# Kernel optimization log

Hardware: AMD Instinct MI355X
Metric: run time of the kernel (lower is better)

The kernel has to match this reference:

```python
import jax, jax.numpy as jnp
import numpy as np

T = 1024          # num tokens
H = 2048          # hidden_size
NH = 16           # attention heads
NKV = 4           # kv heads (GQA)
HD = 128          # head_dim
E = 32            # num routed experts
K = 4             # top_k
I = 1024          # moe_intermediate_size
NS = 1            # num_shared_experts
EPS = 1e-6
THETA = 600000.0  # rope base
SCALE = HD ** -0.5


def rmsnorm(x, w):
    return x * jax.lax.rsqrt(jnp.mean(x * x, axis=-1, keepdims=True) + EPS) * w


def rope(x, positions):
    # x: [T, n_heads, HD], neox-style rotation on full head_dim
    half = HD // 2
    inv_freq = 1.0 / (THETA ** (jnp.arange(half, dtype=jnp.float32) / half))
    ang = positions.astype(jnp.float32)[:, None] * inv_freq        # [T, half]
    cos = jnp.cos(ang)[:, None, :]
    sin = jnp.sin(ang)[:, None, :]
    x1, x2 = x[..., :half], x[..., half:]
    return jnp.concatenate([x1 * cos - x2 * sin, x1 * sin + x2 * cos], axis=-1)


def setup_inputs() -> dict:
    key = jax.random.key(0)
    ks = jax.random.split(key, 10)
    s = 0.02
    return {
        "hidden_states": jax.random.normal(ks[0], (T, H), dtype=jnp.float32),
        "positions": jnp.arange(T, dtype=jnp.int32),
        "w_rms1": jnp.ones((H,), jnp.float32),
        "w_rms2": jnp.ones((H,), jnp.float32),
        "w_qkv": jax.random.normal(ks[1], ((NH + 2 * NKV) * HD, H), jnp.float32) * s,
        "w_o": jax.random.normal(ks[2], (H, NH * HD), jnp.float32) * s,
        "w_router": jax.random.normal(ks[3], (E, H), jnp.float32) * s,
        "w1": jax.random.normal(ks[4], (E, H, I), jnp.float32) * s,   # expert gate proj
        "w3": jax.random.normal(ks[5], (E, H, I), jnp.float32) * s,   # expert up proj
        "w2": jax.random.normal(ks[6], (E, I, H), jnp.float32) * s,   # expert down proj
        "ws_gate_up": jax.random.normal(ks[7], (2 * I * NS, H), jnp.float32) * s,
        "ws_down": jax.random.normal(ks[8], (H, I * NS), jnp.float32) * s,
    }


def reference(hidden_states, positions, w_rms1, w_rms2, w_qkv, w_o, w_router,
              w1, w3, w2, ws_gate_up, ws_down):
    x = hidden_states
    # ---- attention block ----
    h = rmsnorm(x, w_rms1)
    qkv = h @ w_qkv.T                                   # [T, (NH+2NKV)*HD]
    q = qkv[:, : NH * HD].reshape(T, NH, HD)
    k = qkv[:, NH * HD : (NH + NKV) * HD].reshape(T, NKV, HD)
    v = qkv[:, (NH + NKV) * HD :].reshape(T, NKV, HD)
    q = rope(q, positions)
    k = rope(k, positions)
    rep = NH // NKV
    k = jnp.repeat(k, rep, axis=1)                      # [T, NH, HD]
    v = jnp.repeat(v, rep, axis=1)
    scores = jnp.einsum("thd,shd->hts", q, k) * SCALE   # [NH, T, T]
    causal = jnp.tril(jnp.ones((T, T), dtype=bool))
    scores = jnp.where(causal, scores, -jnp.inf)
    attn = jax.nn.softmax(scores, axis=-1)
    o = jnp.einsum("hts,shd->thd", attn, v).reshape(T, NH * HD)
    x = x + o @ w_o.T                                   # residual
    # ---- MoE block ----
    h2 = rmsnorm(x, w_rms2)
    # router in fp32 (router_dtype default)
    logits = h2.astype(jnp.float32) @ w_router.T        # [T, E]
    probs = jax.nn.softmax(logits, axis=-1)
    topv, topi = jax.lax.top_k(probs, K)                # [T, K]
    topv = topv / jnp.sum(topv, axis=-1, keepdims=True)  # norm_topk_prob
    combine = jnp.zeros((T, E), jnp.float32).at[jnp.arange(T)[:, None], topi].add(topv)
    combine = combine.astype(h2.dtype)                  # routed_scaling_factor = 1.0
    g = jnp.einsum("th,ehi->tei", h2, w1)               # [T, E, I]
    u = jnp.einsum("th,ehi->tei", h2, w3)
    a = jax.nn.silu(g) * u                              # SiluAndMul
    d = jnp.einsum("tei,eih->teh", a, w2)               # [T, E, H]
    routed = jnp.einsum("teh,te->th", d, combine)
    # shared expert MLP
    gu = h2 @ ws_gate_up.T                              # [T, 2*I*NS]
    gs, us = gu[:, : I * NS], gu[:, I * NS :]
    shared = (jax.nn.silu(gs) * us) @ ws_down.T
    return x + routed + shared
```

## Files before the change

### kernel.cpp

```cpp
#include <hip/hip_runtime.h>
#include <hip/hip_bf16.h>
#include <math.h>
#include <stdint.h>

#define T_ 1024
#define H_ 2048
#define NH_ 16
#define NKV_ 4
#define HD_ 128
#define E_ 32
#define TOPK_ 4
#define I_ 1024
#define QKVN_ 3072
#define EPS_ 1e-6f
#define THETA_ 600000.0f
#define SCALE_ 0.08838834764831845f

typedef unsigned short u16;
typedef u16 u16x4 __attribute__((ext_vector_type(4)));
typedef u16 u16x8 __attribute__((ext_vector_type(8)));
typedef __bf16 bf16x8 __attribute__((ext_vector_type(8)));
typedef float f32x4 __attribute__((ext_vector_type(4)));

__device__ __forceinline__ u16 f2b(float f) {
  unsigned u = __builtin_bit_cast(unsigned, f);
  u += 0x7FFFu + ((u >> 16) & 1u);
  return (u16)(u >> 16);
}
__device__ __forceinline__ float b2f(u16 x) {
  unsigned u = ((unsigned)x) << 16;
  return __builtin_bit_cast(float, u);
}
__device__ __forceinline__ int s2(int i) { return (i ^ (i >> 2)) & 3; }

__device__ __forceinline__ void gload16(const void* g, void* l) {
  __builtin_amdgcn_global_load_lds(
      reinterpret_cast<const __attribute__((address_space(1))) unsigned int*>(
          reinterpret_cast<uintptr_t>(g)),
      reinterpret_cast<__attribute__((address_space(3))) unsigned int*>(
          reinterpret_cast<uintptr_t>(l)),
      16, 0, 0);
}

template<int EPI, bool GATHER>
__global__ __launch_bounds__(512, 8) void moe_gemm_k(
    const u16* __restrict__ A, const float* __restrict__ B, const float* __restrict__ B2,
    float* __restrict__ O1, float* __restrict__ O2,
    int NW, int lda, int ldb, int kchunk,
    const int* __restrict__ eoff, const int* __restrict__ slots,
    const float* __restrict__ slotw, long long sBz)
{
  __shared__ u16 As[2][64 * 32];
  __shared__ u16 Bs[2][128 * 32];

  const int e = blockIdx.y >> 3;
  const int mb = blockIdx.y & 7;
  const int goff = eoff[e];
  const int Mloc = eoff[e + 1] - goff;
  const int m0 = mb * 64;
  if (m0 >= Mloc) return;

  const int xx = blockIdx.x;
  const float* Bp;
  float* Op;
  int n0;
  if constexpr (EPI == 0) {
    int wsel = xx >> 3;
    n0 = (xx & 7) * 128;
    Bp = (wsel ? B2 : B) + (long long)e * sBz;
    Op = wsel ? O2 : O1;
  } else {
    n0 = xx * 128;
    Bp = B + (long long)e * sBz;
    Op = O1;
  }
  const int k0base = blockIdx.z * kchunk;
  const u16* Ae = GATHER ? A : (A + (long long)goff * lda);

  const int tid = threadIdx.x;
  const int lane = tid & 63;
  const int wv = tid >> 6;
  const int wm = wv >> 2, wn = wv & 3;

  const u16* Abase = nullptr;
  if (wv < 4) {
    int r = wv * 16 + (lane >> 2);
    int rr = m0 + r;
    if (rr > Mloc - 1) rr = Mloc - 1;
    long long grow = GATHER ? (long long)slots[goff + rr] : (long long)rr;
    Abase = Ae + grow * (long long)lda + (((lane & 3) ^ s2(r)) << 3);
  }

  const int bn = tid & 127;
  const int bkc = tid >> 7;
  const float* Bbase = Bp + (long long)(bkc << 3) * ldb + n0 + bn;
  const int bws = bn * 32 + ((bkc ^ s2(bn)) << 3);

  float br[8];
  auto loadB = [&](int k0) {
    const float* p = Bbase + (long long)k0 * ldb;
    #pragma unroll
    for (int j = 0; j < 8; ++j) br[j] = p[(long long)j * ldb];
  };
  auto writeB = [&](int bf) {
    u16x8 o;
    #pragma unroll
    for (int j = 0; j < 8; ++j) o[j] = f2b(br[j]);
    *(u16x8*)(&Bs[bf][bws]) = o;
  };
  auto stageA = [&](int bf, int k0) {
    if (wv < 4) gload16(Abase + k0, &As[bf][wv * 512]);
  };

  f32x4 acc[2][2];
  #pragma unroll
  for (int m = 0; m < 2; ++m)
    #pragma unroll
    for (int n = 0; n < 2; ++n)
      acc[m][n] = f32x4{0.f, 0.f, 0.f, 0.f};

  const int kg = lane >> 4;
  const int cr = lane & 15;

  int aoff[2], boff[2];
  #pragma unroll
  for (int m = 0; m < 2; ++m) {
    int r = wm * 32 + m * 16 + cr;
    aoff[m] = r * 32 + ((kg ^ s2(r)) << 3);
  }
  #pragma unroll
  for (int n = 0; n < 2; ++n) {
    int c = wn * 32 + n * 16 + cr;
    boff[n] = c * 32 + ((kg ^ s2(c)) << 3);
  }

  loadB(k0base);
  stageA(0, k0base);
  writeB(0);
  __syncthreads();

  int buf = 0;
  for (int ks = 0; ks < kchunk; ks += 32) {
    bool more = (ks + 32) < kchunk;
    if (more) { loadB(k0base + ks + 32); stageA(buf ^ 1, k0base + ks + 32); }
    const u16* Ap = &As[buf][0];
    const u16* Bq = &Bs[buf][0];
    bf16x8 af[2], bfr[2];
    #pragma unroll
    for (int m = 0; m < 2; ++m)
      af[m] = __builtin_bit_cast(bf16x8, *(const u16x8*)(Ap + aoff[m]));
    #pragma unroll
    for (int n = 0; n < 2; ++n)
      bfr[n] = __builtin_bit_cast(bf16x8, *(const u16x8*)(Bq + boff[n]));
    #pragma unroll
    for (int m = 0; m < 2; ++m)
      #pragma unroll
      for (int n = 0; n < 2; ++n)
        acc[m][n] = __builtin_amdgcn_mfma_f32_16x16x32_bf16(af[m], bfr[n], acc[m][n], 0, 0, 0);
    if (more) writeB(buf ^ 1);
    __syncthreads();
    buf ^= 1;
  }

  const int rq = lane >> 4;
  #pragma unroll
  for (int m = 0; m < 2; ++m) {
    #pragma unroll
    for (int j = 0; j < 4; ++j) {
      int row = m0 + wm * 32 + m * 16 + rq * 4 + j;
      if (row >= Mloc) continue;
      if constexpr (EPI == 0) {
        float* dst = Op + (long long)(goff + row) * NW;
        #pragma unroll
        for (int n = 0; n < 2; ++n) {
          int col = n0 + wn * 32 + n * 16 + cr;
          dst[col] = acc[m][n][j];
        }
      } else {
        int tok = slots[goff + row];
        float wgt = slotw[goff + row];
        float* dst = Op + (long long)tok * NW;
        #pragma unroll
        for (int n = 0; n < 2; ++n) {
          int col = n0 + wn * 32 + n * 16 + cr;
          atomicAdd(dst + col, wgt * acc[m][n][j]);
        }
      }
    }
  }
}

template<typename TB, int EPI, int CAUSAL>
__global__ __launch_bounds__(512, 8) void dense_gemm_k(
    const u16* __restrict__ A, const TB* __restrict__ B,
    u16* __restrict__ Cb, float* __restrict__ Cf,
    const float* __restrict__ res1, const float* __restrict__ res2,
    int K, int lda, int ldb, int ldc, float alpha,
    long long sAz, long long sBz, long long sCz, int bdivz)
{
  __shared__ u16 As[2][64 * 32];
  __shared__ u16 Bs[2][128 * 32];

  const int m0 = blockIdx.y * 64;
  const int n0 = blockIdx.x * 128;
  if (CAUSAL == 1 && n0 > m0 + 63) return;
  const long long z = blockIdx.z;
  const u16* Ae = A + z * sAz;
  const TB* Be = B + (long long)(z / bdivz) * sBz;
  u16* Cwb = Cb ? Cb + z * sCz : nullptr;

  int kend = K;
  if (CAUSAL == 2) { int ke = m0 + 64; if (ke < kend) kend = ke; }

  const int tid = threadIdx.x;
  const int lane = tid & 63;
  const int wv = tid >> 6;
  const int wm = wv >> 2, wn = wv & 3;

  const u16* Abase = nullptr;
  if (wv < 4) {
    int r = wv * 16 + (lane >> 2);
    Abase = Ae + (long long)(m0 + r) * lda + (((lane & 3) ^ s2(r)) << 3);
  }
  auto stageA = [&](int bf, int k0) {
    if (wv < 4) gload16(Abase + k0, &As[bf][wv * 512]);
  };

  const u16* Bu16base = nullptr;
  const float* Bf32base = nullptr;
  int bws = 0;
  if constexpr (sizeof(TB) == 2) {
    int r = wv * 16 + (lane >> 2);
    Bu16base = (const u16*)Be + (long long)(n0 + r) * ldb + (((lane & 3) ^ s2(r)) << 3);
  } else {
    int bn = tid >> 2, bkq = tid & 3;
    Bf32base = (const float*)Be + (long long)(n0 + bn) * ldb + (bkq << 3);
    bws = bn * 32 + ((bkq ^ s2(bn)) << 3);
  }
  float br[8];
  auto loadB = [&](int k0) {
    const float* p = Bf32base + k0;
    float4 a = *(const float4*)p;
    float4 b = *(const float4*)(p + 4);
    br[0] = a.x; br[1] = a.y; br[2] = a.z; br[3] = a.w;
    br[4] = b.x; br[5] = b.y; br[6] = b.z; br[7] = b.w;
  };
  auto writeB = [&](int bf) {
    u16x8 o;
    #pragma unroll
    for (int j = 0; j < 8; ++j) o[j] = f2b(br[j]);
    *(u16x8*)(&Bs[bf][bws]) = o;
  };
  auto stageBu = [&](int bf, int k0) {
    gload16(Bu16base + k0, &Bs[bf][wv * 512]);
  };

  f32x4 acc[2][2];
  #pragma unroll
  for (int m = 0; m < 2; ++m)
    #pragma unroll
    for (int n = 0; n < 2; ++n)
      acc[m][n] = f32x4{0.f, 0.f, 0.f, 0.f};

  const int kg = lane >> 4;
  const int cr = lane & 15;

  int aoff[2], boff[2];
  #pragma unroll
  for (int m = 0; m < 2; ++m) {
    int r = wm * 32 + m * 16 + cr;
    aoff[m] = r * 32 + ((kg ^ s2(r)) << 3);
  }
  #pragma unroll
  for (int n = 0; n < 2; ++n) {
    int c = wn * 32 + n * 16 + cr;
    boff[n] = c * 32 + ((kg ^ s2(c)) << 3);
  }

  if constexpr (sizeof(TB) == 4) {
    loadB(0); stageA(0, 0); writeB(0);
  } else {
    stageA(0, 0); stageBu(0, 0);
  }
  __syncthreads();

  int buf = 0;
  for (int ks = 0; ks < kend; ks += 32) {
    bool more = (ks + 32) < kend;
    if (more) {
      if constexpr (sizeof(TB) == 4) { loadB(ks + 32); stageA(buf ^ 1, ks + 32); }
      else { stageA(buf ^ 1, ks + 32); stageBu(buf ^ 1, ks + 32); }
    }
    const u16* Ap = &As[buf][0];
    const u16* Bq = &Bs[buf][0];
    bf16x8 af[2], bfr[2];
    #pragma unroll
    for (int m = 0; m < 2; ++m)
      af[m] = __builtin_bit_cast(bf16x8, *(const u16x8*)(Ap + aoff[m]));
    #pragma unroll
    for (int n = 0; n < 2; ++n)
      bfr[n] = __builtin_bit_cast(bf16x8, *(const u16x8*)(Bq + boff[n]));
    #pragma unroll
    for (int m = 0; m < 2; ++m)
      #pragma unroll
      for (int n = 0; n < 2; ++n)
        acc[m][n] = __builtin_amdgcn_mfma_f32_16x16x32_bf16(af[m], bfr[n], acc[m][n], 0, 0, 0);
    if constexpr (sizeof(TB) == 4) { if (more) writeB(buf ^ 1); }
    __syncthreads();
    buf ^= 1;
  }

  const int rq = lane >> 4;
  #pragma unroll
  for (int m = 0; m < 2; ++m) {
    #pragma unroll
    for (int j = 0; j < 4; ++j) {
      int row = m0 + wm * 32 + m * 16 + rq * 4 + j;
      #pragma unroll
      for (int n = 0; n < 2; ++n) {
        int col = n0 + wn * 32 + n * 16 + cr;
        float v = acc[m][n][j];
        long long o = (long long)row * ldc + col;
        if constexpr (EPI == 0) {
          Cwb[o] = f2b(v);
        } else if constexpr (EPI == 1) {
          Cwb[o] = f2b(v * alpha);
        } else if constexpr (EPI == 2) {
          Cf[o] = res1[o] + v;
        } else {
          Cf[o] = res1[o] + res2[o] + v;
        }
      }
    }
  }
}

__global__ __launch_bounds__(256) void vtrans_k(const u16* __restrict__ v_r,
                                                u16* __restrict__ v_t) {
  __shared__ u16 t[64][72];
  int kv = blockIdx.z;
  int s0 = blockIdx.x * 64, d0 = blockIdx.y * 64;
  int tid = threadIdx.x;
  int sr = tid >> 2, dq = (tid & 3) * 16;
  const u16* src = v_r + ((long long)kv * T_ + s0 + sr) * HD_ + d0 + dq;
  *(u16x8*)&t[sr][dq] = *(const u16x8*)src;
  *(u16x8*)&t[sr][dq + 8] = *(const u16x8*)(src + 8);
  __syncthreads();
  int dr = tid >> 2, sq = (tid & 3) * 16;
  u16* dst = v_t + ((long long)kv * HD_ + d0 + dr) * T_ + s0 + sq;
  u16x8 o0, o1;
  #pragma unroll
  for (int j = 0; j < 8; ++j) { o0[j] = t[sq + j][dr]; o1[j] = t[sq + 8 + j][dr]; }
  *(u16x8*)dst = o0;
  *(u16x8*)(dst + 8) = o1;
}

__global__ __launch_bounds__(256) void rmsnorm_k(const float* __restrict__ x,
                                                 const float* __restrict__ w,
                                                 u16* __restrict__ outb,
                                                 float* __restrict__ outf) {
  int t = blockIdx.x;
  int tid = threadIdx.x;
  const float* xr = x + (long long)t * H_;
  float4 a = *(const float4*)(xr + tid * 8);
  float4 b = *(const float4*)(xr + tid * 8 + 4);
  float ss = a.x * a.x + a.y * a.y + a.z * a.z + a.w * a.w +
             b.x * b.x + b.y * b.y + b.z * b.z + b.w * b.w;
  #pragma unroll
  for (int o = 32; o; o >>= 1) ss += __shfl_down(ss, o);
  __shared__ float red[4];
  if ((tid & 63) == 0) red[tid >> 6] = ss;
  __syncthreads();
  float sc = rsqrtf((red[0] + red[1] + red[2] + red[3]) * (1.0f / H_) + EPS_);
  float vo[8] = {a.x, a.y, a.z, a.w, b.x, b.y, b.z, b.w};
  const float* wr = w + tid * 8;
  u16x8 ob;
  #pragma unroll
  for (int q = 0; q < 8; ++q) {
    float val = vo[q] * sc * wr[q];
    ob[q] = f2b(val);
    if (outf) outf[(long long)t * H_ + tid * 8 + q] = val;
  }
  *(u16x8*)(outb + (long long)t * H_ + tid * 8) = ob;
}

__global__ __launch_bounds__(256) void rope_k(const u16* __restrict__ qkv,
                                              const int* __restrict__ pos,
                                              u16* __restrict__ q_r,
                                              u16* __restrict__ k_r,
                                              u16* __restrict__ v_r) {
  int t = blockIdx.x;
  int tid = threadIdx.x;
  float p = (float)pos[t];
  const u16* row = qkv + (long long)t * QKVN_;
  const float cfac = logf(THETA_) * (1.0f / 64.0f);
  #pragma unroll
  for (int it = 0; it < 4; ++it) {
    int item = it * 256 + tid;
    int h = item >> 6, d = item & 63;
    float inv = expf(-cfac * (float)d);
    float ang = p * inv;
    float c = cosf(ang), s = sinf(ang);
    float x1v = b2f(row[h * 128 + d]);
    float x2v = b2f(row[h * 128 + 64 + d]);
    u16* dst = q_r + ((long long)h * T_ + t) * HD_;
    dst[d] = f2b(x1v * c - x2v * s);
    dst[d + 64] = f2b(x1v * s + x2v * c);
  }
  {
    int item = tid;
    int kv = item >> 6, d = item & 63;
    float inv = expf(-cfac * (float)d);
    float ang = p * inv;
    float c = cosf(ang), s = sinf(ang);
    float x1v = b2f(row[NH_ * HD_ + kv * 128 + d]);
    float x2v = b2f(row[NH_ * HD_ + kv * 128 + 64 + d]);
    u16* dst = k_r + ((long long)kv * T_ + t) * HD_;
    dst[d] = f2b(x1v * c - x2v * s);
    dst[d + 64] = f2b(x1v * s + x2v * c);
  }
  #pragma unroll
  for (int it = 0; it < 2; ++it) {
    int item = it * 256 + tid;
    int kv = item >> 7, d = item & 127;
    v_r[((long long)kv * T_ + t) * HD_ + d] = row[(NH_ + NKV_) * HD_ + kv * 128 + d];
  }
}

__global__ __launch_bounds__(64) void softmax_k(u16* __restrict__ P) {
  int r = blockIdx.x;
  int h = r >> 10, i = r & 1023;
  u16* row = P + ((long long)h * T_ + i) * T_;
  int lane = threadIdx.x;
  int n = i + 1;
  float vals[16];
  float mx = -1e30f;
  #pragma unroll
  for (int it = 0; it < 16; ++it) {
    int j = it * 64 + lane;
    float s = (j < n) ? b2f(row[j]) : -1e30f;
    vals[it] = s;
    mx = fmaxf(mx, s);
  }
  #pragma unroll
  for (int o = 32; o; o >>= 1) mx = fmaxf(mx, __shfl_xor(mx, o));
  float sum = 0.f;
  #pragma unroll
  for (int it = 0; it < 16; ++it) {
    int j = it * 64 + lane;
    float e = (j < n) ? __expf(vals[it] - mx) : 0.f;
    vals[it] = e;
    sum += e;
  }
  #pragma unroll
  for (int o = 32; o; o >>= 1) sum += __shfl_xor(sum, o);
  float inv = 1.f / sum;
  #pragma unroll
  for (int it = 0; it < 16; ++it) {
    int j = it * 64 + lane;
    row[j] = f2b(vals[it] * inv);
  }
}

__global__ __launch_bounds__(64) void router_k(const float* __restrict__ h2,
                                               const float* __restrict__ wr,
                                               float* __restrict__ logits) {
  int b = blockIdx.x;
  int t = b >> 5, e = b & 31;
  const float* xr = h2 + (long long)t * H_;
  const float* wv = wr + (long long)e * H_;
  int lane = threadIdx.x;
  float s = 0.f;
  #pragma unroll
  for (int it = 0; it < 8; ++it) {
    int h = it * 256 + lane * 4;
    float4 a = *(const float4*)(xr + h);
    float4 w4 = *(const float4*)(wv + h);
    s += a.x * w4.x + a.y * w4.y + a.z * w4.z + a.w * w4.w;
  }
  #pragma unroll
  for (int o = 32; o; o >>= 1) s += __shfl_xor(s, o);
  if (lane == 0) logits[b] = s;
}

__global__ __launch_bounds__(256) void topk_k(const float* __restrict__ logits,
                                              int* __restrict__ topi,
                                              float* __restrict__ topw) {
  int t = blockIdx.x * 256 + threadIdx.x;
  if (t >= T_) return;
  float l[E_];
  #pragma unroll
  for (int e = 0; e < E_; ++e) l[e] = logits[t * E_ + e];
  int sel[TOPK_];
  float sv[TOPK_];
  unsigned used = 0;
  for (int j = 0; j < TOPK_; ++j) {
    float best = -1e30f;
    int bi = 0;
    for (int e = 0; e < E_; ++e) {
      if (used & (1u << e)) continue;
      if (l[e] > best) { best = l[e]; bi = e; }
    }
    used |= 1u << bi;
    sel[j] = bi;
    sv[j] = best;
  }
  float mx = sv[0];
  float s = 0.f;
  #pragma unroll
  for (int j = 0; j < TOPK_; ++j) { sv[j] = __expf(sv[j] - mx); s += sv[j]; }
  float inv = 1.f / s;
  #pragma unroll
  for (int j = 0; j < TOPK_; ++j) {
    topi[t * TOPK_ + j] = sel[j];
    topw[t * TOPK_ + j] = sv[j] * inv;
  }
}

__global__ __launch_bounds__(256) void hist_k(const int* __restrict__ topi, int* __restrict__ cnt) {
  int idx = blockIdx.x * 256 + threadIdx.x;
  if (idx < T_ * TOPK_) atomicAdd(&cnt[topi[idx]], 1);
}

__global__ __launch_bounds__(64) void scan_k(const int* __restrict__ cnt,
                                             int* __restrict__ eoff,
                                             int* __restrict__ cursor) {
  if (threadIdx.x == 0) {
    int s = 0;
    for (int e = 0; e < E_; ++e) { eoff[e] = s; cursor[e] = s; s += cnt[e]; }
    eoff[E_] = s;
  }
}

__global__ __launch_bounds__(256) void scatter_k(const int* __restrict__ topi,
                                                 const float* __restrict__ topw,
                                                 int* __restrict__ cursor,
                                                 int* __restrict__ slots,
                                                 float* __restrict__ slotw) {
  int idx = blockIdx.x * 256 + threadIdx.x;
  if (idx >= T_ * TOPK_) return;
  int e = topi[idx];
  int pos = atomicAdd(&cursor[e], 1);
  slots[pos] = idx >> 2;
  slotw[pos] = topw[idx];
}

__global__ __launch_bounds__(256) void silumul_f_k(const float* __restrict__ g,
                                                   const float* __restrict__ u,
                                                   u16* __restrict__ a) {
  long long idx = ((long long)blockIdx.x * 256 + threadIdx.x) * 8;
  float4 g0 = *(const float4*)(g + idx);
  float4 g1 = *(const float4*)(g + idx + 4);
  float4 u0 = *(const float4*)(u + idx);
  float4 u1 = *(const float4*)(u + idx + 4);
  float gv[8] = {g0.x, g0.y, g0.z, g0.w, g1.x, g1.y, g1.z, g1.w};
  float uv[8] = {u0.x, u0.y, u0.z, u0.w, u1.x, u1.y, u1.z, u1.w};
  u16x8 o;
  #pragma unroll
  for (int q = 0; q < 8; ++q) {
    float x = gv[q];
    float sl = x / (1.f + __expf(-x));
    o[q] = f2b(sl * uv[q]);
  }
  *(u16x8*)(a + idx) = o;
}

__global__ __launch_bounds__(256) void sharedact_k(const u16* __restrict__ gu,
                                                   u16* __restrict__ act) {
  long long idx = ((long long)blockIdx.x * 256 + threadIdx.x) * 8;
  long long t = idx >> 10;
  int i = (int)(idx & 1023);
  const u16* row = gu + t * (2 * I_);
  u16x8 g = *(const u16x8*)(row + i);
  u16x8 u = *(const u16x8*)(row + I_ + i);
  u16x8 o;
  #pragma unroll
  for (int q = 0; q < 8; ++q) {
    float x = b2f(g[q]);
    float y = b2f(u[q]);
    float sl = x / (1.f + __expf(-x));
    o[q] = f2b(sl * y);
  }
  *(u16x8*)(act + t * I_ + i) = o;
}

extern "C" void kernel_launch(void* const* d_in, const int* in_sizes, int n_in,
                              void* d_out, int out_size, void* d_ws, size_t ws_size,
                              hipStream_t stream) {
  const float* x        = (const float*)d_in[0];
  const int* positions  = (const int*)d_in[1];
  const float* w_rms1   = (const float*)d_in[2];
  const float* w_rms2   = (const float*)d_in[3];
  const float* w_qkv    = (const float*)d_in[4];
  const float* w_o      = (const float*)d_in[5];
  const float* w_router = (const float*)d_in[6];
  const float* w1       = (const float*)d_in[7];
  const float* w3       = (const float*)d_in[8];
  const float* w2       = (const float*)d_in[9];
  const float* ws_gu    = (const float*)d_in[10];
  const float* ws_dn    = (const float*)d_in[11];
  float* out = (float*)d_out;

  char* ws = (char*)d_ws;
  size_t off = 0;
  auto alloc = [&](size_t bytes) {
    size_t o = off;
    off = (off + bytes + 255) & ~(size_t)255;
    return (void*)(ws + o);
  };
  u16*  h1b     = (u16*)alloc((size_t)T_ * H_ * 2);
  u16*  qkvb    = (u16*)alloc((size_t)T_ * QKVN_ * 2);
  u16*  q_r     = (u16*)alloc((size_t)NH_ * T_ * HD_ * 2);
  u16*  k_r     = (u16*)alloc((size_t)NKV_ * T_ * HD_ * 2);
  u16*  v_r     = (u16*)alloc((size_t)NKV_ * T_ * HD_ * 2);
  u16*  v_t     = (u16*)alloc((size_t)NKV_ * HD_ * T_ * 2);
  u16*  scoresP = (u16*)alloc((size_t)NH_ * T_ * T_ * 2);
  u16*  o_attn  = (u16*)alloc((size_t)T_ * H_ * 2);
  float* x1     = (float*)alloc((size_t)T_ * H_ * 4);
  float* h2f    = (float*)alloc((size_t)T_ * H_ * 4);
  u16*  h2b     = (u16*)alloc((size_t)T_ * H_ * 2);
  u16*  gub     = (u16*)alloc((size_t)T_ * 2 * I_ * 2);
  u16*  actsh   = (u16*)alloc((size_t)T_ * I_ * 2);
  float* logits = (float*)alloc((size_t)T_ * E_ * 4);
  int*  topi    = (int*)alloc((size_t)T_ * TOPK_ * 4);
  float* topw   = (float*)alloc((size_t)T_ * TOPK_ * 4);
  int*  cnt     = (int*)alloc(E_ * 4);
  int*  eoffp   = (int*)alloc((E_ + 1) * 4);
  int*  cursor  = (int*)alloc(E_ * 4);
  int*  slots   = (int*)alloc((size_t)T_ * TOPK_ * 4);
  float* slotw  = (float*)alloc((size_t)T_ * TOPK_ * 4);
  u16*  a_g     = (u16*)alloc((size_t)T_ * TOPK_ * I_ * 2);
  float* routed = (float*)alloc((size_t)T_ * H_ * 4);

  float* g_f32 = (float*)scoresP;
  float* u_f32 = g_f32 + (size_t)T_ * TOPK_ * I_;

  hipMemsetAsync(routed, 0, (size_t)T_ * H_ * 4, stream);
  hipMemsetAsync(cnt, 0, E_ * 4, stream);

  rmsnorm_k<<<T_, 256, 0, stream>>>(x, w_rms1, h1b, nullptr);

  dense_gemm_k<float, 0, 0><<<dim3(24, 16, 1), 512, 0, stream>>>(
      h1b, w_qkv, qkvb, nullptr, nullptr, nullptr,
      H_, H_, H_, QKVN_, 1.f, 0, 0, 0, 1);

  rope_k<<<T_, 256, 0, stream>>>(qkvb, positions, q_r, k_r, v_r);
  vtrans_k<<<dim3(16, 2, 4), 256, 0, stream>>>(v_r, v_t);

  dense_gemm_k<u16, 1, 1><<<dim3(8, 16, NH_), 512, 0, stream>>>(
      q_r, k_r, scoresP, nullptr, nullptr, nullptr,
      HD_, HD_, HD_, T_, SCALE_,
      (long long)T_ * HD_, (long long)T_ * HD_, (long long)T_ * T_, NH_ / NKV_);

  softmax_k<<<NH_ * T_, 64, 0, stream>>>(scoresP);

  dense_gemm_k<u16, 0, 2><<<dim3(1, 16, NH_), 512, 0, stream>>>(
      scoresP, v_t, o_attn, nullptr, nullptr, nullptr,
      T_, T_, T_, H_, 1.f,
      (long long)T_ * T_, (long long)HD_ * T_, (long long)HD_, NH_ / NKV_);

  dense_gemm_k<float, 2, 0><<<dim3(16, 16, 1), 512, 0, stream>>>(
      o_attn, w_o, nullptr, x1, x, nullptr,
      H_, H_, H_, H_, 1.f, 0, 0, 0, 1);

  rmsnorm_k<<<T_, 256, 0, stream>>>(x1, w_rms2, h2b, h2f);

  router_k<<<T_ * E_, 64, 0, stream>>>(h2f, w_router, logits);
  topk_k<<<4, 256, 0, stream>>>(logits, topi, topw);
  hist_k<<<16, 256, 0, stream>>>(topi, cnt);
  scan_k<<<1, 64, 0, stream>>>(cnt, eoffp, cursor);
  scatter_k<<<16, 256, 0, stream>>>(topi, topw, cursor, slots, slotw);

  moe_gemm_k<0, true><<<dim3(16, E_ * 8, 1), 512, 0, stream>>>(
      h2b, w1, w3, g_f32, u_f32,
      I_, H_, I_, H_, eoffp, slots, nullptr, (long long)H_ * I_);
  silumul_f_k<<<(T_ * TOPK_ * I_) / (256 * 8), 256, 0, stream>>>(g_f32, u_f32, a_g);

  moe_gemm_k<1, false><<<dim3(16, E_ * 8, 1), 512, 0, stream>>>(
      a_g, w2, nullptr, routed, nullptr,
      H_, I_, H_, I_, eoffp, slots, slotw, (long long)I_ * H_);

  dense_gemm_k<float, 0, 0><<<dim3(16, 16, 1), 512, 0, stream>>>(
      h2b, ws_gu, gub, nullptr, nullptr, nullptr,
      H_, H_, H_, 2 * I_, 1.f, 0, 0, 0, 1);
  sharedact_k<<<(T_ * I_) / (256 * 8), 256, 0, stream>>>(gub, actsh);

  dense_gemm_k<float, 4, 0><<<dim3(16, 16, 1), 512, 0, stream>>>(
      actsh, ws_dn, nullptr, out, x1, routed,
      I_, I_, I_, H_, 1.f, 0, 0, 0, 1);
}
```

Before: 616.0 us.

## Use persistent work-queue scheduling over compacted expert tiles in MoE GEMMs

Replaces the fixed grid over all experts and 8 row blocks, where most blocks exit early, with a persistent grid of 1024 blocks. Each block claims tile indices from an atomic counter. The scan kernel now also builds a prefix sum of per-expert tile counts, and a binary search maps each claimed tile to its expert and row block. This removes launches of empty blocks and balances uneven expert loads, at the cost of two barriers and an atomic per tile plus an extra counter memset.

```diff
diff --git a/kernel.cpp b/kernel.cpp
--- a/kernel.cpp
+++ b/kernel.cpp
@@ -46,144 +46,156 @@
 __global__ __launch_bounds__(512, 8) void moe_gemm_k(
     const u16* __restrict__ A, const float* __restrict__ B, const float* __restrict__ B2,
     float* __restrict__ O1, float* __restrict__ O2,
-    int NW, int lda, int ldb, int kchunk,
-    const int* __restrict__ eoff, const int* __restrict__ slots,
-    const float* __restrict__ slotw, long long sBz)
+    int NW, int lda, int ldb, int K, int nx,
+    const int* __restrict__ eoff, const int* __restrict__ tpre,
+    const int* __restrict__ slots, const float* __restrict__ slotw,
+    long long sBz, int* __restrict__ ctr)
 {
   __shared__ u16 As[2][64 * 32];
   __shared__ u16 Bs[2][128 * 32];
-
-  const int e = blockIdx.y >> 3;
-  const int mb = blockIdx.y & 7;
-  const int goff = eoff[e];
-  const int Mloc = eoff[e + 1] - goff;
-  const int m0 = mb * 64;
-  if (m0 >= Mloc) return;
-
-  const int xx = blockIdx.x;
-  const float* Bp;
-  float* Op;
-  int n0;
-  if constexpr (EPI == 0) {
-    int wsel = xx >> 3;
-    n0 = (xx & 7) * 128;
-    Bp = (wsel ? B2 : B) + (long long)e * sBz;
-    Op = wsel ? O2 : O1;
-  } else {
-    n0 = xx * 128;
-    Bp = B + (long long)e * sBz;
-    Op = O1;
-  }
-  const int k0base = blockIdx.z * kchunk;
-  const u16* Ae = GATHER ? A : (A + (long long)goff * lda);
+  __shared__ int sh_idx;
 
   const int tid = threadIdx.x;
   const int lane = tid & 63;
   const int wv = tid >> 6;
   const int wm = wv >> 2, wn = wv & 3;
-
-  const u16* Abase = nullptr;
-  if (wv < 4) {
-    int r = wv * 16 + (lane >> 2);
-    int rr = m0 + r;
-    if (rr > Mloc - 1) rr = Mloc - 1;
-    long long grow = GATHER ? (long long)slots[goff + rr] : (long long)rr;
-    Abase = Ae + grow * (long long)lda + (((lane & 3) ^ s2(r)) << 3);
-  }
-
-  const int bn = tid & 127;
-  const int bkc = tid >> 7;
-  const float* Bbase = Bp + (long long)(bkc << 3) * ldb + n0 + bn;
-  const int bws = bn * 32 + ((bkc ^ s2(bn)) << 3);
-
-  float br[8];
-  auto loadB = [&](int k0) {
-    const float* p = Bbase + (long long)k0 * ldb;
-    #pragma unroll
-    for (int j = 0; j < 8; ++j) br[j] = p[(long long)j * ldb];
-  };
-  auto writeB = [&](int bf) {
-    u16x8 o;
-    #pragma unroll
-    for (int j = 0; j < 8; ++j) o[j] = f2b(br[j]);
-    *(u16x8*)(&Bs[bf][bws]) = o;
-  };
-  auto stageA = [&](int bf, int k0) {
-    if (wv < 4) gload16(Abase + k0, &As[bf][wv * 512]);
-  };
-
-  f32x4 acc[2][2];
-  #pragma unroll
-  for (int m = 0; m < 2; ++m)
-    #pragma unroll
-    for (int n = 0; n < 2; ++n)
-      acc[m][n] = f32x4{0.f, 0.f, 0.f, 0.f};
-
   const int kg = lane >> 4;
   const int cr = lane & 15;
 
-  int aoff[2], boff[2];
-  #pragma unroll
-  for (int m = 0; m < 2; ++m) {
-    int r = wm * 32 + m * 16 + cr;
-    aoff[m] = r * 32 + ((kg ^ s2(r)) << 3);
-  }
-  #pragma unroll
-  for (int n = 0; n < 2; ++n) {
-    int c = wn * 32 + n * 16 + cr;
-    boff[n] = c * 32 + ((kg ^ s2(c)) << 3);
-  }
-
-  loadB(k0base);
-  stageA(0, k0base);
-  writeB(0);
-  __syncthreads();
-
-  int buf = 0;
-  for (int ks = 0; ks < kchunk; ks += 32) {
-    bool more = (ks + 32) < kchunk;
-    if (more) { loadB(k0base + ks + 32); stageA(buf ^ 1, k0base + ks + 32); }
-    const u16* Ap = &As[buf][0];
-    const u16* Bq = &Bs[buf][0];
-    bf16x8 af[2], bfr[2];
+  const int total = tpre[E_] * nx;
+
+  for (;;) {
+    if (tid == 0) sh_idx = atomicAdd(ctr, 1);
+    __syncthreads();
+    const int idx = sh_idx;
+    __syncthreads();
+    if (idx >= total) return;
+
+    const int t = idx / nx;
+    const int xx = idx - t * nx;
+    int lo = 0, hi = E_;
+    while (hi - lo > 1) { int mid = (lo + hi) >> 1; if (tpre[mid] <= t) lo = mid; else hi = mid; }
+    const int e = lo;
+    const int mb = t - tpre[e];
+    const int goff = eoff[e];
+    const int Mloc = eoff[e + 1] - goff;
+    const int m0 = mb * 64;
+
+    const float* Bp;
+    float* Op;
+    int n0;
+    if constexpr (EPI == 0) {
+      int wsel = xx >> 3;
+      n0 = (xx & 7) * 128;
+      Bp = (wsel ? B2 : B) + (long long)e * sBz;
+      Op = wsel ? O2 : O1;
+    } else {
+      n0 = xx * 128;
+      Bp = B + (long long)e * sBz;
+      Op = O1;
+    }
+    const u16* Ae = GATHER ? A : (A + (long long)goff * lda);
+
+    const u16* Abase = nullptr;
+    if (wv < 4) {
+      int r = wv * 16 + (lane >> 2);
+      int rr = m0 + r;
+      if (rr > Mloc - 1) rr = Mloc - 1;
+      long long grow = GATHER ? (long long)slots[goff + rr] : (long long)rr;
+      Abase = Ae + grow * (long long)lda + (((lane & 3) ^ s2(r)) << 3);
+    }
+
+    const int bn = tid & 127;
+    const int bkc = tid >> 7;
+    const float* Bbase = Bp + (long long)(bkc << 3) * ldb + n0 + bn;
+    const int bws = bn * 32 + ((bkc ^ s2(bn)) << 3);
+
+    float br[8];
+    auto loadB = [&](int k0) {
+      const float* p = Bbase + (long long)k0 * ldb;
+      #pragma unroll
+      for (int j = 0; j < 8; ++j) br[j] = p[(long long)j * ldb];
+    };
+    auto writeB = [&](int bf) {
+      u16x8 o;
+      #pragma unroll
+      for (int j = 0; j < 8; ++j) o[j] = f2b(br[j]);
+      *(u16x8*)(&Bs[bf][bws]) = o;
+    };
+    auto stageA = [&](int bf, int k0) {
+      if (wv < 4) gload16(Abase + k0, &As[bf][wv * 512]);
+    };
+
+    f32x4 acc[2][2];
     #pragma unroll
     for (int m = 0; m < 2; ++m)
-      af[m] = __builtin_bit_cast(bf16x8, *(const u16x8*)(Ap + aoff[m]));
-    #pragma unroll
-    for (int n = 0; n < 2; ++n)
-      bfr[n] = __builtin_bit_cast(bf16x8, *(const u16x8*)(Bq + boff[n]));
-    #pragma unroll
-    for (int m = 0; m < 2; ++m)
       #pragma unroll
       for (int n = 0; n < 2; ++n)
-        acc[m][n] = __builtin_amdgcn_mfma_f32_16x16x32_bf16(af[m], bfr[n], acc[m][n], 0, 0, 0);
-    if (more) writeB(buf ^ 1);
+        acc[m][n] = f32x4{0.f, 0.f, 0.f, 0.f};
+
+    int aoff[2], boff[2];
+    #pragma unroll
+    for (int m = 0; m < 2; ++m) {
+      int r = wm * 32 + m * 16 + cr;
+      aoff[m] = r * 32 + ((kg ^ s2(r)) << 3);
+    }
+    #pragma unroll
+    for (int n = 0; n < 2; ++n) {
+      int c = wn * 32 + n * 16 + cr;
+      boff[n] = c * 32 + ((kg ^ s2(c)) << 3);
+    }
+
+    loadB(0);
+    stageA(0, 0);
+    writeB(0);
     __syncthreads();
-    buf ^= 1;
-  }
-
-  const int rq = lane >> 4;
-  #pragma unroll
-  for (int m = 0; m < 2; ++m) {
-    #pragma unroll
-    for (int j = 0; j < 4; ++j) {
-      int row = m0 + wm * 32 + m * 16 + rq * 4 + j;
-      if (row >= Mloc) continue;
-      if constexpr (EPI == 0) {
-        float* dst = Op + (long long)(goff + row) * NW;
+
+    int buf = 0;
+    for (int ks = 0; ks < K; ks += 32) {
+      bool more = (ks + 32) < K;
+      if (more) { loadB(ks + 32); stageA(buf ^ 1, ks + 32); }
+      const u16* Ap = &As[buf][0];
+      const u16* Bq = &Bs[buf][0];
+      bf16x8 af[2], bfr[2];
+      #pragma unroll
+      for (int m = 0; m < 2; ++m)
+        af[m] = __builtin_bit_cast(bf16x8, *(const u16x8*)(Ap + aoff[m]));
+      #pragma unroll
+      for (int n = 0; n < 2; ++n)
+        bfr[n] = __builtin_bit_cast(bf16x8, *(const u16x8*)(Bq + boff[n]));
+      #pragma unroll
+      for (int m = 0; m < 2; ++m)
         #pragma unroll
-        for (int n = 0; n < 2; ++n) {
-          int col = n0 + wn * 32 + n * 16 + cr;
-          dst[col] = acc[m][n][j];
-        }
-      } else {
-        int tok = slots[goff + row];
-        float wgt = slotw[goff + row];
-        float* dst = Op + (long long)tok * NW;
-        #pragma unroll
-        for (int n = 0; n < 2; ++n) {
-          int col = n0 + wn * 32 + n * 16 + cr;
-          atomicAdd(dst + col, wgt * acc[m][n][j]);
+        for (int n = 0; n < 2; ++n)
+          acc[m][n] = __builtin_amdgcn_mfma_f32_16x16x32_bf16(af[m], bfr[n], acc[m][n], 0, 0, 0);
+      if (more) writeB(buf ^ 1);
+      __syncthreads();
+      buf ^= 1;
+    }
+
+    const int rq = lane >> 4;
+    #pragma unroll
+    for (int m = 0; m < 2; ++m) {
+      #pragma unroll
+      for (int j = 0; j < 4; ++j) {
+        int row = m0 + wm * 32 + m * 16 + rq * 4 + j;
+        if (row >= Mloc) continue;
+        if constexpr (EPI == 0) {
+          float* dst = Op + (long long)(goff + row) * NW;
+          #pragma unroll
+          for (int n = 0; n < 2; ++n) {
+            int col = n0 + wn * 32 + n * 16 + cr;
+            dst[col] = acc[m][n][j];
+          }
+        } else {
+          int tok = slots[goff + row];
+          float wgt = slotw[goff + row];
+          float* dst = Op + (long long)tok * NW;
+          #pragma unroll
+          for (int n = 0; n < 2; ++n) {
+            int col = n0 + wn * 32 + n * 16 + cr;
+            atomicAdd(dst + col, wgt * acc[m][n][j]);
+          }
         }
       }
     }
@@ -524,11 +536,16 @@
 
 __global__ __launch_bounds__(64) void scan_k(const int* __restrict__ cnt,
                                              int* __restrict__ eoff,
-                                             int* __restrict__ cursor) {
+                                             int* __restrict__ cursor,
+                                             int* __restrict__ tpre) {
   if (threadIdx.x == 0) {
-    int s = 0;
-    for (int e = 0; e < E_; ++e) { eoff[e] = s; cursor[e] = s; s += cnt[e]; }
-    eoff[E_] = s;
+    int s = 0, tt = 0;
+    for (int e = 0; e < E_; ++e) {
+      eoff[e] = s; cursor[e] = s; tpre[e] = tt;
+      tt += (cnt[e] + 63) >> 6;
+      s += cnt[e];
+    }
+    eoff[E_] = s; tpre[E_] = tt;
   }
 }
 
@@ -627,6 +644,8 @@
   int*  cnt     = (int*)alloc(E_ * 4);
   int*  eoffp   = (int*)alloc((E_ + 1) * 4);
   int*  cursor  = (int*)alloc(E_ * 4);
+  int*  tpre    = (int*)alloc((E_ + 1) * 4);
+  int*  wqctr   = (int*)alloc(2 * 4);
   int*  slots   = (int*)alloc((size_t)T_ * TOPK_ * 4);
   float* slotw  = (float*)alloc((size_t)T_ * TOPK_ * 4);
   u16*  a_g     = (u16*)alloc((size_t)T_ * TOPK_ * I_ * 2);
@@ -637,6 +656,7 @@
 
   hipMemsetAsync(routed, 0, (size_t)T_ * H_ * 4, stream);
   hipMemsetAsync(cnt, 0, E_ * 4, stream);
+  hipMemsetAsync(wqctr, 0, 2 * 4, stream);
 
   rmsnorm_k<<<T_, 256, 0, stream>>>(x, w_rms1, h1b, nullptr);
 
@@ -668,17 +688,19 @@
   router_k<<<T_ * E_, 64, 0, stream>>>(h2f, w_router, logits);
   topk_k<<<4, 256, 0, stream>>>(logits, topi, topw);
   hist_k<<<16, 256, 0, stream>>>(topi, cnt);
-  scan_k<<<1, 64, 0, stream>>>(cnt, eoffp, cursor);
+  scan_k<<<1, 64, 0, stream>>>(cnt, eoffp, cursor, tpre);
   scatter_k<<<16, 256, 0, stream>>>(topi, topw, cursor, slots, slotw);
 
-  moe_gemm_k<0, true><<<dim3(16, E_ * 8, 1), 512, 0, stream>>>(
+  moe_gemm_k<0, true><<<1024, 512, 0, stream>>>(
       h2b, w1, w3, g_f32, u_f32,
-      I_, H_, I_, H_, eoffp, slots, nullptr, (long long)H_ * I_);
+      I_, H_, I_, H_, 16, eoffp, tpre, slots, nullptr,
+      (long long)H_ * I_, wqctr);
   silumul_f_k<<<(T_ * TOPK_ * I_) / (256 * 8), 256, 0, stream>>>(g_f32, u_f32, a_g);
 
-  moe_gemm_k<1, false><<<dim3(16, E_ * 8, 1), 512, 0, stream>>>(
+  moe_gemm_k<1, false><<<1024, 512, 0, stream>>>(
       a_g, w2, nullptr, routed, nullptr,
-      H_, I_, H_, I_, eoffp, slots, slotw, (long long)I_ * H_);
+      H_, I_, H_, I_, 16, eoffp, tpre, slots, slotw,
+      (long long)I_ * H_, wqctr + 1);
 
   dense_gemm_k<float, 0, 0><<<dim3(16, 16, 1), 512, 0, stream>>>(
       h2b, ws_gu, gub, nullptr, nullptr, nullptr,
```

After: 668.3 us. 8.5% more time.
